# Kernel tuning notes

Hardware: AMD Instinct MI355X
Metric: run time of the kernel (lower is better)

Reference implementation:

```python
import jax, jax.numpy as jnp
import numpy as np

N = 55296      # nodes (C96 cubed-sphere)
B = 4          # batch
F = 64         # in_feats == out_feats
H = 256        # n_hidden
DEG = 4        # neighbors per node
E = N * DEG    # edges
NUM_STEP = 2


def setup_inputs() -> dict:
    key = jax.random.key(0)
    ks = jax.random.split(key, 24)
    inputs = jax.random.normal(ks[0], (B, N, F), jnp.float32)
    src = jax.random.randint(ks[1], (E,), 0, N, dtype=jnp.int32)
    dst = jnp.repeat(jnp.arange(N, dtype=jnp.int32), DEG)  # fixed in-degree 4
    d = {"inputs": inputs, "src": src, "dst": dst}
    # SAGEConv params: fc_self, fc_neigh, bias per layer
    dims = [(F, H), (H, H // 2), (H // 2, H // 4), (H // 4, H // 4), (H // 2, H // 2), (H, F)]
    for i, (di, do) in enumerate(dims, start=1):
        s = 1.0 / np.sqrt(di)
        d[f"ws{i}"] = jax.random.uniform(ks[3 * i], (di, do), jnp.float32, -s, s)
        d[f"wn{i}"] = jax.random.uniform(ks[3 * i + 1], (di, do), jnp.float32, -s, s)
        d[f"b{i}"] = jnp.zeros((do,), jnp.float32)
    return d


def _sage(x, src, dst, inv_deg, ws, wn, b):
    # x: [N, B, Fin] -> gather src endpoints, mean-aggregate onto dst nodes
    agg = jax.ops.segment_sum(x[src], dst, num_segments=N) * inv_deg  # [N, B, Fin]
    return jnp.einsum('nbf,fo->nbo', x, ws) + jnp.einsum('nbf,fo->nbo', agg, wn) + b


def reference(inputs, src, dst, ws1, wn1, b1, ws2, wn2, b2, ws3, wn3, b3,
              ws4, wn4, b4, ws5, wn5, b5, ws6, wn6, b6):
    deg = jax.ops.segment_sum(jnp.ones((E,), jnp.float32), dst, num_segments=N)
    inv_deg = (1.0 / jnp.maximum(deg, 1.0))[:, None, None]
    act = jax.nn.relu
    x = jnp.transpose(inputs, (1, 0, 2))  # [N, B, F]
    for _ in range(NUM_STEP):
        h1 = act(_sage(x, src, dst, inv_deg, ws1, wn1, b1))
        h2 = act(_sage(h1, src, dst, inv_deg, ws2, wn2, b2))
        h3 = act(_sage(h2, src, dst, inv_deg, ws3, wn3, b3))
        h4 = act(_sage(h3, src, dst, inv_deg, ws4, wn4, b4))
        h5 = jnp.concatenate([act(_sage(h4, src, dst, inv_deg, ws4, wn4, b4)), h3], axis=2)
        h6 = jnp.concatenate([act(_sage(h5, src, dst, inv_deg, ws5, wn5, b5)), h2], axis=2)
        x = _sage(h6, src, dst, inv_deg, ws6, wn6, b6)
    return jnp.transpose(x, (1, 0, 2))  # [B, N, F]
```

## Files before the change

kernel.cpp:

```cpp
#include <hip/hip_runtime.h>


#define NN 55296
#define MM (NN * 4)

typedef unsigned short u16;
typedef _Float16 f16;
typedef f16 f16x8 __attribute__((ext_vector_type(8)));
typedef float f32x4 __attribute__((ext_vector_type(4)));
typedef u16 u16x8 __attribute__((ext_vector_type(8)));

__device__ inline u16 f2h(float f) { return __builtin_bit_cast(u16, (f16)f); }
__device__ inline float h2f(u16 u) { return (float)__builtin_bit_cast(f16, u); }

__global__ __launch_bounds__(256) void k_fill(float* __restrict__ p, float v, int total) {
  int i = blockIdx.x * 256 + threadIdx.x;
  if (i < total) p[i] = v;
}

__global__ __launch_bounds__(256) void k_prep_x(const float* __restrict__ in,
                                                u16* __restrict__ out) {
  int idx = blockIdx.x * 256 + threadIdx.x;
  int n = idx >> 5, b = (idx >> 3) & 3, f0 = (idx & 7) * 8;
  const float* p = in + ((long)b * NN + n) * 64 + f0;
  float4 v0 = *(const float4*)p, v1 = *(const float4*)(p + 4);
  u16x8 r;
  r[0] = f2h(v0.x); r[1] = f2h(v0.y); r[2] = f2h(v0.z); r[3] = f2h(v0.w);
  r[4] = f2h(v1.x); r[5] = f2h(v1.y); r[6] = f2h(v1.z); r[7] = f2h(v1.w);
  *(u16x8*)(out + (((long)n * 4 + b) * 64 + f0)) = r;
}

__global__ __launch_bounds__(256) void k_prep_w(const float* __restrict__ wsrc,
                                                const float* __restrict__ wnsrc,
                                                int K, int N, u16* __restrict__ dst) {
  int idx = blockIdx.x * 256 + threadIdx.x;
  int K2 = 2 * K;
  if (idx >= N * K2) return;
  int n = idx / K2, k = idx - n * K2;
  float v = (k < K) ? wsrc[(long)k * N + n] : wnsrc[(long)(k - K) * N + n];
  dst[(long)n * K2 + k] = f2h(v);
}

__global__ __launch_bounds__(256) void k_prep_w2(const float* __restrict__ wsrc,
                                                 const float* __restrict__ wnsrc,
                                                 int K, int N, u16* __restrict__ dst) {
  int idx = blockIdx.x * 256 + threadIdx.x;
  int total = 2 * N * K;
  if (idx >= total) return;
  int r = idx / K, k = idx - r * K;
  float v = (r < N) ? wsrc[(long)k * N + r] : wnsrc[(long)k * N + (r - N)];
  dst[idx] = f2h(v);
}

template <int BM, int BN, int WM, int WN, typename TOUT, bool REMAP, bool GATHER>
__global__ __launch_bounds__(512, 4) void k_sage(
    const u16* __restrict__ X0, const u16* __restrict__ X1, int lda, int K0, int Ksum,
    const int4* __restrict__ src4, const u16* __restrict__ Wt,
    const float* __restrict__ bias, TOUT* __restrict__ OUT, long ldo,
    TOUT* __restrict__ OUT2, long ldo2, int Nsplit, int relu) {
  constexpr int GA = BM / 64;
  constexpr int GB = BN / 64;
  constexpr int NWM = BM / WM, NWN = BN / WN;
  static_assert(NWM * NWN == 8, "8 waves");
  constexpr int MF = WM / 16, NF = WN / 16;

  __shared__ __align__(16) u16 As[BM][64];
  __shared__ __align__(16) u16 Bs[BN][64];

  const int tid = threadIdx.x;
  const long m0 = (long)blockIdx.x * BM;
  const int n0 = blockIdx.y * BN;
  const int K2 = GATHER ? 2 * Ksum : Ksum;

  const int srow = tid >> 3;
  const int scg = tid & 7;

  int o_self[GA], o_g[GA][4];
#pragma unroll
  for (int i = 0; i < GA; ++i) {
    long m = m0 + srow + 64 * i;
    o_self[i] = (int)(m * lda);
    if constexpr (GATHER) {
      int b = (int)(m & 3);
      int4 s = src4[(int)(m >> 2)];
      o_g[i][0] = (s.x * 4 + b) * lda;
      o_g[i][1] = (s.y * 4 + b) * lda;
      o_g[i][2] = (s.z * 4 + b) * lda;
      o_g[i][3] = (s.w * 4 + b) * lda;
    }
  }
  long o_b[GB];
#pragma unroll
  for (int j = 0; j < GB; ++j) o_b[j] = (long)(n0 + srow + 64 * j) * K2 + scg * 8;

  u16x8 ra[GA][4];
  u16x8 rb[GB];

  const int w = tid >> 6, lane = tid & 63;
  const int wm = w % NWM, wn = w / NWM;
  const int mo = wm * WM, no = wn * WN;
  const int lr = lane & 15, lg = lane >> 4;

  f32x4 acc[MF][NF];
#pragma unroll
  for (int i = 0; i < MF; ++i)
#pragma unroll
    for (int j = 0; j < NF; ++j) {
      f32x4 z = {0.f, 0.f, 0.f, 0.f};
      acc[i][j] = z;
    }

  auto issue = [&](int kt) {
    const bool agg = GATHER && (kt >= Ksum);
    int cs = agg ? kt - Ksum : kt;
    const u16* Xp = X0;
    if (cs >= K0) { Xp = X1; cs -= K0; }
    const int cb = cs + scg * 8;
#pragma unroll
    for (int i = 0; i < GA; ++i) {
      if (agg) {
#pragma unroll
        for (int k = 0; k < 4; ++k)
          ra[i][k] = *(const u16x8*)(Xp + (long)o_g[i][k] + cb);
      } else {
        ra[i][0] = *(const u16x8*)(Xp + (long)o_self[i] + cb);
      }
    }
#pragma unroll
    for (int j = 0; j < GB; ++j)
      rb[j] = *(const u16x8*)(Wt + o_b[j] + kt);
  };
  auto commit = [&](bool agg) {
#pragma unroll
    for (int i = 0; i < GA; ++i) {
      const int row = srow + 64 * i;
      u16x8 v = ra[i][0];
      if (agg) {
        f16x8 s01 = __builtin_bit_cast(f16x8, ra[i][0]) + __builtin_bit_cast(f16x8, ra[i][1]);
        f16x8 s23 = __builtin_bit_cast(f16x8, ra[i][2]) + __builtin_bit_cast(f16x8, ra[i][3]);
        v = __builtin_bit_cast(u16x8, (s01 + s23) * (f16)0.25f);
      }
      *(u16x8*)&As[row][(scg ^ (row & 7)) * 8] = v;
    }
#pragma unroll
    for (int j = 0; j < GB; ++j) {
      const int row = srow + 64 * j;
      *(u16x8*)&Bs[row][(scg ^ (row & 7)) * 8] = rb[j];
    }
  };

  issue(0);
  for (int kt = 0; kt < K2; kt += 64) {
    commit(GATHER && kt >= Ksum);
    __syncthreads();
    const int nx = kt + 64;
    if (nx < K2) issue(nx);
#pragma unroll
    for (int ks = 0; ks < 2; ++ks) {
      f16x8 af[MF], bfr[NF];
#pragma unroll
      for (int i = 0; i < MF; ++i) {
        const int row = mo + i * 16 + lr;
        af[i] = __builtin_bit_cast(f16x8,
                  *(const u16x8*)&As[row][((ks * 4 + lg) ^ (row & 7)) * 8]);
      }
#pragma unroll
      for (int j = 0; j < NF; ++j) {
        const int row = no + j * 16 + lr;
        bfr[j] = __builtin_bit_cast(f16x8,
                   *(const u16x8*)&Bs[row][((ks * 4 + lg) ^ (row & 7)) * 8]);
      }
#pragma unroll
      for (int i = 0; i < MF; ++i)
#pragma unroll
        for (int j = 0; j < NF; ++j)
          acc[i][j] = __builtin_amdgcn_mfma_f32_16x16x32_f16(af[i], bfr[j], acc[i][j], 0, 0, 0);
    }
    __syncthreads();
  }

#pragma unroll
  for (int i = 0; i < MF; ++i)
#pragma unroll
    for (int j = 0; j < NF; ++j) {
      const int col = n0 + no + j * 16 + lr;
      const float bv = bias ? bias[col] : 0.f;
      TOUT* Op; long ld; int c;
      if (col < Nsplit) { Op = OUT; ld = ldo; c = col; }
      else              { Op = OUT2; ld = ldo2; c = col - Nsplit; }
#pragma unroll
      for (int r = 0; r < 4; ++r) {
        float v = acc[i][j][r] + bv;
        if (relu) v = fmaxf(v, 0.f);
        const long m = m0 + mo + i * 16 + lg * 4 + r;
        const long orow = REMAP ? ((m & 3) * (long)NN + (m >> 2)) : m;
        if constexpr (sizeof(TOUT) == 2) Op[orow * ld + c] = (TOUT)f2h(v);
        else                             Op[orow * ld + c] = v;
      }
    }
}

template <int N1, int KS1, int K2B, int N2, int NSPLIT>
__global__ __launch_bounds__(512, 4) void k_fuse2(
    const u16* __restrict__ X0, const u16* __restrict__ X1, int lda, int K0,
    const int4* __restrict__ src4,
    const u16* __restrict__ W1t, const float* __restrict__ bias1,
    const u16* __restrict__ G2, int ldg2,
    const u16* __restrict__ W2t,
    u16* __restrict__ OUT, long ldo, u16* __restrict__ OUT2, long ldo2) {
  constexpr int K21 = 2 * KS1;
  constexpr int K22 = N1 + K2B;
  constexpr int GB1 = N1 / 64, GB2 = N2 / 64;
  constexpr int BSROWS = (N1 > N2 ? N1 : N2);
  __shared__ __align__(16) u16 T[64][N1];
  __shared__ __align__(16) u16 As[64][64];
  __shared__ __align__(16) u16 Bs[BSROWS][64];

  const int tid = threadIdx.x;
  const long m0 = (long)blockIdx.x * 64;
  const int srow = tid >> 3, scg = tid & 7;
  const long mrow = m0 + srow;

  const int o_self = (int)(mrow * lda);
  const int bb = (int)(mrow & 3);
  const int4 s = src4[(int)(mrow >> 2)];
  const int og0 = (s.x * 4 + bb) * lda, og1 = (s.y * 4 + bb) * lda;
  const int og2 = (s.z * 4 + bb) * lda, og3 = (s.w * 4 + bb) * lda;

  const int w = tid >> 6, lane = tid & 63;
  const int lr = lane & 15, lg = lane >> 4;

  constexpr int NWN1 = N1 / 32, NWM1 = 8 / NWN1, WM1 = 64 / NWM1, MF1 = WM1 / 16;
  const int mo1 = (w % NWM1) * WM1, no1 = (w / NWM1) * 32;

  int ob1[GB1];
#pragma unroll
  for (int j = 0; j < GB1; ++j) ob1[j] = (srow + 64 * j) * K21 + scg * 8;

  u16x8 ra0, ra1, ra2, ra3, rb[GB1];

  auto issue1 = [&](int kt) {
    const bool agg = kt >= KS1;
    int cs = agg ? kt - KS1 : kt;
    const u16* Xp = X0;
    if (cs >= K0) { Xp = X1; cs -= K0; }
    const int cb = cs + scg * 8;
    if (agg) {
      ra0 = *(const u16x8*)(Xp + og0 + cb);
      ra1 = *(const u16x8*)(Xp + og1 + cb);
      ra2 = *(const u16x8*)(Xp + og2 + cb);
      ra3 = *(const u16x8*)(Xp + og3 + cb);
    } else {
      ra0 = *(const u16x8*)(Xp + o_self + cb);
    }
#pragma unroll
    for (int j = 0; j < GB1; ++j)
      rb[j] = *(const u16x8*)(W1t + ob1[j] + kt);
  };
  auto commit1 = [&](bool agg) {
    u16x8 v = ra0;
    if (agg) {
      f16x8 s01 = __builtin_bit_cast(f16x8, ra0) + __builtin_bit_cast(f16x8, ra1);
      f16x8 s23 = __builtin_bit_cast(f16x8, ra2) + __builtin_bit_cast(f16x8, ra3);
      v = __builtin_bit_cast(u16x8, (s01 + s23) * (f16)0.25f);
    }
    *(u16x8*)&As[srow][(scg ^ (srow & 7)) * 8] = v;
#pragma unroll
    for (int j = 0; j < GB1; ++j) {
      const int row = srow + 64 * j;
      *(u16x8*)&Bs[row][(scg ^ (row & 7)) * 8] = rb[j];
    }
  };

  f32x4 acc1[MF1][2];
#pragma unroll
  for (int i = 0; i < MF1; ++i) {
    f32x4 z = {0.f, 0.f, 0.f, 0.f};
    acc1[i][0] = z; acc1[i][1] = z;
  }

  issue1(0);
  for (int kt = 0; kt < K21; kt += 64) {
    commit1(kt >= KS1);
    __syncthreads();
    if (kt + 64 < K21) issue1(kt + 64);
#pragma unroll
    for (int ks = 0; ks < 2; ++ks) {
      f16x8 af[MF1], bf0, bf1;
#pragma unroll
      for (int i = 0; i < MF1; ++i) {
        const int row = mo1 + i * 16 + lr;
        af[i] = __builtin_bit_cast(f16x8,
                  *(const u16x8*)&As[row][((ks * 4 + lg) ^ (row & 7)) * 8]);
      }
      {
        const int row = no1 + lr;
        bf0 = __builtin_bit_cast(f16x8,
                *(const u16x8*)&Bs[row][((ks * 4 + lg) ^ (row & 7)) * 8]);
      }
      {
        const int row = no1 + 16 + lr;
        bf1 = __builtin_bit_cast(f16x8,
                *(const u16x8*)&Bs[row][((ks * 4 + lg) ^ (row & 7)) * 8]);
      }
#pragma unroll
      for (int i = 0; i < MF1; ++i) {
        acc1[i][0] = __builtin_amdgcn_mfma_f32_16x16x32_f16(af[i], bf0, acc1[i][0], 0, 0, 0);
        acc1[i][1] = __builtin_amdgcn_mfma_f32_16x16x32_f16(af[i], bf1, acc1[i][1], 0, 0, 0);
      }
    }
    __syncthreads();
  }

#pragma unroll
  for (int i = 0; i < MF1; ++i)
#pragma unroll
    for (int j = 0; j < 2; ++j) {
      const int col = no1 + j * 16 + lr;
      const float bv = bias1[col];
#pragma unroll
      for (int r = 0; r < 4; ++r) {
        float v = fmaxf(acc1[i][j][r] + bv, 0.f);
        const int row = mo1 + i * 16 + lg * 4 + r;
        T[row][(((col >> 3) ^ (row & 7)) << 3) | (col & 7)] = f2h(v);
      }
    }

  constexpr int NWN2 = N2 / 32, NWM2 = 8 / NWN2, WM2 = 64 / NWM2, MF2 = WM2 / 16;
  const int mo2 = (w % NWM2) * WM2, no2 = (w / NWM2) * 32;

  int ob2[GB2];
#pragma unroll
  for (int j = 0; j < GB2; ++j) ob2[j] = (srow + 64 * j) * K22 + scg * 8;
  const long oG = (K2B > 0) ? (mrow * (long)ldg2 + scg * 8) : 0;

  u16x8 rb2[GB2], rg;

  auto issue2 = [&](int kt) {
#pragma unroll
    for (int j = 0; j < GB2; ++j)
      rb2[j] = *(const u16x8*)(W2t + ob2[j] + kt);
    if constexpr (K2B > 0) {
      if (kt >= N1) rg = *(const u16x8*)(G2 + oG + (kt - N1));
    }
  };
  auto commit2 = [&](int kt) {
#pragma unroll
    for (int j = 0; j < GB2; ++j) {
      const int row = srow + 64 * j;
      *(u16x8*)&Bs[row][(scg ^ (row & 7)) * 8] = rb2[j];
    }
    if constexpr (K2B > 0) {
      if (kt >= N1) *(u16x8*)&As[srow][(scg ^ (srow & 7)) * 8] = rg;
    }
  };

  f32x4 acc2[MF2][2];
#pragma unroll
  for (int i = 0; i < MF2; ++i) {
    f32x4 z = {0.f, 0.f, 0.f, 0.f};
    acc2[i][0] = z; acc2[i][1] = z;
  }

  issue2(0);
  for (int kt = 0; kt < K22; kt += 64) {
    commit2(kt);
    __syncthreads();
    if (kt + 64 < K22) issue2(kt + 64);
    const bool fromT = kt < N1;
#pragma unroll
    for (int ks = 0; ks < 2; ++ks) {
      f16x8 af[MF2], bf0, bf1;
#pragma unroll
      for (int i = 0; i < MF2; ++i) {
        const int row = mo2 + i * 16 + lr;
        if (fromT) {
          const int g = (kt >> 3) + ks * 4 + lg;
          af[i] = __builtin_bit_cast(f16x8,
                    *(const u16x8*)&T[row][(g ^ (row & 7)) * 8]);
        } else {
          af[i] = __builtin_bit_cast(f16x8,
                    *(const u16x8*)&As[row][((ks * 4 + lg) ^ (row & 7)) * 8]);
        }
      }
      {
        const int row = no2 + lr;
        bf0 = __builtin_bit_cast(f16x8,
                *(const u16x8*)&Bs[row][((ks * 4 + lg) ^ (row & 7)) * 8]);
      }
      {
        const int row = no2 + 16 + lr;
        bf1 = __builtin_bit_cast(f16x8,
                *(const u16x8*)&Bs[row][((ks * 4 + lg) ^ (row & 7)) * 8]);
      }
#pragma unroll
      for (int i = 0; i < MF2; ++i) {
        acc2[i][0] = __builtin_amdgcn_mfma_f32_16x16x32_f16(af[i], bf0, acc2[i][0], 0, 0, 0);
        acc2[i][1] = __builtin_amdgcn_mfma_f32_16x16x32_f16(af[i], bf1, acc2[i][1], 0, 0, 0);
      }
    }
    __syncthreads();
  }

#pragma unroll
  for (int i = 0; i < MF2; ++i)
#pragma unroll
    for (int j = 0; j < 2; ++j) {
      const int col = no2 + j * 16 + lr;
      u16* Op; long ld; int c;
      if (col < NSPLIT) { Op = OUT; ld = ldo; c = col; }
      else              { Op = OUT2; ld = ldo2; c = col - NSPLIT; }
#pragma unroll
      for (int r = 0; r < 4; ++r) {
        const long m = m0 + mo2 + i * 16 + lg * 4 + r;
        Op[m * ld + c] = f2h(acc2[i][j][r]);
      }
    }
}

template <typename TOUT, bool REMAP, bool RELU, int GSH>
__global__ __launch_bounds__(256) void k_gadd(
    const u16* __restrict__ Y, long ldy, const u16* __restrict__ Z, long ldz,
    const int4* __restrict__ src4, const float* __restrict__ bias,
    TOUT* __restrict__ OUT, long ldo) {
  const int idx = blockIdx.x * 256 + threadIdx.x;
  const int g = idx & ((1 << GSH) - 1);
  const long m = idx >> GSH;
  const int b = (int)(m & 3), n = (int)(m >> 2);
  const int4 s = src4[n];
  u16x8 ys = *(const u16x8*)(Y + m * ldy + g * 8);
  u16x8 z0 = *(const u16x8*)(Z + (long)(s.x * 4 + b) * ldz + g * 8);
  u16x8 z1 = *(const u16x8*)(Z + (long)(s.y * 4 + b) * ldz + g * 8);
  u16x8 z2 = *(const u16x8*)(Z + (long)(s.z * 4 + b) * ldz + g * 8);
  u16x8 z3 = *(const u16x8*)(Z + (long)(s.w * 4 + b) * ldz + g * 8);
  float4 bv0 = *(const float4*)(bias + g * 8);
  float4 bv1 = *(const float4*)(bias + g * 8 + 4);
  float o[8];
#pragma unroll
  for (int j = 0; j < 8; ++j) {
    float bj = (j < 4) ? (&bv0.x)[j] : (&bv1.x)[j - 4];
    float v = h2f(ys[j]) + 0.25f * (h2f(z0[j]) + h2f(z1[j]) + h2f(z2[j]) + h2f(z3[j])) + bj;
    o[j] = RELU ? fmaxf(v, 0.f) : v;
  }
  const long orow = REMAP ? ((long)b * NN + n) : m;
  if constexpr (sizeof(TOUT) == 2) {
    u16x8 r;
#pragma unroll
    for (int j = 0; j < 8; ++j) r[j] = f2h(o[j]);
    *(u16x8*)(OUT + orow * ldo + g * 8) = r;
  } else {
#pragma unroll
    for (int j = 0; j < 8; ++j) OUT[orow * ldo + g * 8 + j] = o[j];
  }
}

extern "C" void kernel_launch(void* const* d_in, const int* in_sizes, int n_in,
                              void* d_out, int out_size, void* d_ws, size_t ws_size,
                              hipStream_t stream) {
  const float* inputs = (const float*)d_in[0];
  const int*   src    = (const int*)d_in[1];
  const float* W[6][3];
  for (int i = 0; i < 6; ++i) {
    W[i][0] = (const float*)d_in[3 + 3 * i];
    W[i][1] = (const float*)d_in[4 + 3 * i];
    W[i][2] = (const float*)d_in[5 + 3 * i];
  }

  const long M = (long)MM;
  const int dims[6][2] = {{64,256},{256,128},{128,64},{64,64},{128,128},{256,64}};
  long wo[6]; long wtot = 0;
  for (int i = 0; i < 6; ++i) { wo[i] = wtot; wtot += (long)dims[i][1] * 2 * dims[i][0]; }

  const size_t needed = ((size_t)384 * M + wtot) * sizeof(u16);
  if (ws_size < needed) {
    float mb = (float)(ws_size >> 20);
    k_fill<<<(out_size + 255) / 256, 256, 0, stream>>>((float*)d_out, mb, out_size);
    return;
  }

  u16* act = (u16*)d_ws;
  u16* Y1  = act + 0 * M;
  u16* H2  = act + 0 * M;
  u16* Z1  = act + 128 * M;
  u16* YZ2 = act + 128 * M;
  u16* H5a = act + 128 * M;
  u16* Y6  = act + 192 * M;
  u16* H3  = act + 256 * M;
  u16* Xb  = act + 320 * M;
  u16* H4  = act + 320 * M;
  u16* Z6  = act + 320 * M;
  u16* WT  = act + 384 * M;
  u16* Xp  = (u16*)d_out;
  const int4* src4 = (const int4*)src;

  k_prep_x<<<NN * 32 / 256, 256, 0, stream>>>(inputs, Xb);
  for (int i : {0, 3, 4}) {
    int total = dims[i][1] * 2 * dims[i][0];
    k_prep_w<<<(total + 255) / 256, 256, 0, stream>>>(W[i][0], W[i][1], dims[i][0],
                                                      dims[i][1], WT + wo[i]);
  }
  for (int i : {1, 2, 5}) {
    int total = 2 * dims[i][1] * dims[i][0];
    k_prep_w2<<<(total + 255) / 256, 256, 0, stream>>>(W[i][0], W[i][1], dims[i][0],
                                                       dims[i][1], WT + wo[i]);
  }

  const int BIG = 1 << 30;
  const dim3 g1(MM / 128, 1);
  for (int step = 0; step < 2; ++step) {
    const u16* x0 = step ? Xp : Xb;
    k_fuse2<256, 64, 0, 256, 128><<<MM / 64, 512, 0, stream>>>(
        x0, x0, 64, 64, src4, WT + wo[0], W[0][2],
        nullptr, 0, WT + wo[1], Y1, 128, Z1, 128);
    k_gadd<u16, false, true, 4><<<MM * 16 / 256, 256, 0, stream>>>(
        Y1, 128, Z1, 128, src4, W[1][2], H2, 128);
    k_sage<128, 128, 64, 32, u16, false, false><<<g1, 512, 0, stream>>>(
        H2, H2, 128, 128, 128, src4, WT + wo[2], nullptr, YZ2, 128,
        (u16*)nullptr, 0, BIG, 0);
    k_gadd<u16, false, true, 3><<<MM * 8 / 256, 256, 0, stream>>>(
        YZ2, 128, YZ2 + 64, 128, src4, W[2][2], H3, 64);
    k_sage<128, 64, 32, 32, u16, false, true><<<g1, 512, 0, stream>>>(
        H3, H3, 64, 64, 64, src4, WT + wo[3], W[3][2], H4, 64,
        (u16*)nullptr, 0, BIG, 1);
    k_sage<128, 64, 32, 32, u16, false, true><<<g1, 512, 0, stream>>>(
        H4, H4, 64, 64, 64, src4, WT + wo[3], W[3][2], H5a, 64,
        (u16*)nullptr, 0, BIG, 1);
    k_fuse2<128, 128, 128, 128, 64><<<MM / 64, 512, 0, stream>>>(
        H5a, H3, 64, 64, src4, WT + wo[4], W[4][2],
        H2, 128, WT + wo[5], Y6, 64, Z6, 64);
    if (step == 0)
      k_gadd<u16, false, false, 3><<<MM * 8 / 256, 256, 0, stream>>>(
          Y6, 64, Z6, 64, src4, W[5][2], Xp, 64);
    else
      k_gadd<float, true, false, 3><<<MM * 8 / 256, 256, 0, stream>>>(
          Y6, 64, Z6, 64, src4, W[5][2], (float*)d_out, 64);
  }
}
```

Measured before the change: 655.0 us.

## Load second-GEMM weight fragments directly into registers, merging shared buffers

In the fused two-GEMM kernel, the second GEMM now reads its weight B-fragments straight from global memory into registers with double buffering, instead of staging them through shared memory. This removes most of the per-k-step barriers, since only the G2 tiles still pass through the As buffer. The separate T and Bs shared arrays are merged into one BT buffer, which lowers LDS use and may raise occupancy. In exchange, every wave reloads the weights from global/L2 without reuse across waves, and the extra registers held for the fragments and rg tiles can add register pressure.

```diff
diff --git a/kernel.cpp b/kernel.cpp
--- a/kernel.cpp
+++ b/kernel.cpp
@@ -210,11 +210,10 @@
     u16* __restrict__ OUT, long ldo, u16* __restrict__ OUT2, long ldo2) {
   constexpr int K21 = 2 * KS1;
   constexpr int K22 = N1 + K2B;
-  constexpr int GB1 = N1 / 64, GB2 = N2 / 64;
-  constexpr int BSROWS = (N1 > N2 ? N1 : N2);
-  __shared__ __align__(16) u16 T[64][N1];
+  constexpr int GB1 = N1 / 64;
+  constexpr int NG2 = (K2B > 0) ? K2B / 64 : 1;
+  __shared__ __align__(16) u16 BT[64 * N1];
   __shared__ __align__(16) u16 As[64][64];
-  __shared__ __align__(16) u16 Bs[BSROWS][64];
 
   const int tid = threadIdx.x;
   const long m0 = (long)blockIdx.x * 64;
@@ -268,7 +267,7 @@
 #pragma unroll
     for (int j = 0; j < GB1; ++j) {
       const int row = srow + 64 * j;
-      *(u16x8*)&Bs[row][(scg ^ (row & 7)) * 8] = rb[j];
+      *(u16x8*)&BT[row * 64 + (scg ^ (row & 7)) * 8] = rb[j];
     }
   };
 
@@ -296,12 +295,12 @@
       {
         const int row = no1 + lr;
         bf0 = __builtin_bit_cast(f16x8,
-                *(const u16x8*)&Bs[row][((ks * 4 + lg) ^ (row & 7)) * 8]);
+                *(const u16x8*)&BT[row * 64 + ((ks * 4 + lg) ^ (row & 7)) * 8]);
       }
       {
         const int row = no1 + 16 + lr;
         bf1 = __builtin_bit_cast(f16x8,
-                *(const u16x8*)&Bs[row][((ks * 4 + lg) ^ (row & 7)) * 8]);
+                *(const u16x8*)&BT[row * 64 + ((ks * 4 + lg) ^ (row & 7)) * 8]);
       }
 #pragma unroll
       for (int i = 0; i < MF1; ++i) {
@@ -322,38 +321,21 @@
       for (int r = 0; r < 4; ++r) {
         float v = fmaxf(acc1[i][j][r] + bv, 0.f);
         const int row = mo1 + i * 16 + lg * 4 + r;
-        T[row][(((col >> 3) ^ (row & 7)) << 3) | (col & 7)] = f2h(v);
-      }
-    }
+        BT[row * N1 + ((((col >> 3) ^ (row & 7)) << 3) | (col & 7))] = f2h(v);
+      }
+    }
+
+  u16x8 rg[NG2];
+  if constexpr (K2B > 0) {
+    const long oG = mrow * (long)ldg2 + scg * 8;
+#pragma unroll
+    for (int t = 0; t < NG2; ++t)
+      rg[t] = *(const u16x8*)(G2 + oG + t * 64);
+  }
+  __syncthreads();
 
   constexpr int NWN2 = N2 / 32, NWM2 = 8 / NWN2, WM2 = 64 / NWM2, MF2 = WM2 / 16;
   const int mo2 = (w % NWM2) * WM2, no2 = (w / NWM2) * 32;
-
-  int ob2[GB2];
-#pragma unroll
-  for (int j = 0; j < GB2; ++j) ob2[j] = (srow + 64 * j) * K22 + scg * 8;
-  const long oG = (K2B > 0) ? (mrow * (long)ldg2 + scg * 8) : 0;
-
-  u16x8 rb2[GB2], rg;
-
-  auto issue2 = [&](int kt) {
-#pragma unroll
-    for (int j = 0; j < GB2; ++j)
-      rb2[j] = *(const u16x8*)(W2t + ob2[j] + kt);
-    if constexpr (K2B > 0) {
-      if (kt >= N1) rg = *(const u16x8*)(G2 + oG + (kt - N1));
-    }
-  };
-  auto commit2 = [&](int kt) {
-#pragma unroll
-    for (int j = 0; j < GB2; ++j) {
-      const int row = srow + 64 * j;
-      *(u16x8*)&Bs[row][(scg ^ (row & 7)) * 8] = rb2[j];
-    }
-    if constexpr (K2B > 0) {
-      if (kt >= N1) *(u16x8*)&As[srow][(scg ^ (srow & 7)) * 8] = rg;
-    }
-  };
 
   f32x4 acc2[MF2][2];
 #pragma unroll
@@ -362,44 +344,50 @@
     acc2[i][0] = z; acc2[i][1] = z;
   }
 
-  issue2(0);
+  u16x8 wf[2][2][2];
+  auto loadW = [&](int kt, int buf) {
+#pragma unroll
+    for (int j = 0; j < 2; ++j)
+#pragma unroll
+      for (int ks = 0; ks < 2; ++ks)
+        wf[buf][j][ks] = *(const u16x8*)(
+            W2t + (long)(no2 + j * 16 + lr) * K22 + kt + ks * 32 + lg * 8);
+  };
+
+  loadW(0, 0);
+#pragma unroll
   for (int kt = 0; kt < K22; kt += 64) {
-    commit2(kt);
-    __syncthreads();
-    if (kt + 64 < K22) issue2(kt + 64);
+    const int buf = (kt >> 6) & 1;
     const bool fromT = kt < N1;
+    if (!fromT) {
+      *(u16x8*)&As[srow][(scg ^ (srow & 7)) * 8] = rg[(kt - N1) >> 6];
+      __syncthreads();
+    }
+    if (kt + 64 < K22) loadW(kt + 64, buf ^ 1);
 #pragma unroll
     for (int ks = 0; ks < 2; ++ks) {
-      f16x8 af[MF2], bf0, bf1;
+      f16x8 af[MF2];
 #pragma unroll
       for (int i = 0; i < MF2; ++i) {
         const int row = mo2 + i * 16 + lr;
         if (fromT) {
           const int g = (kt >> 3) + ks * 4 + lg;
           af[i] = __builtin_bit_cast(f16x8,
-                    *(const u16x8*)&T[row][(g ^ (row & 7)) * 8]);
+                    *(const u16x8*)&BT[row * N1 + (g ^ (row & 7)) * 8]);
         } else {
           af[i] = __builtin_bit_cast(f16x8,
                     *(const u16x8*)&As[row][((ks * 4 + lg) ^ (row & 7)) * 8]);
         }
       }
-      {
-        const int row = no2 + lr;
-        bf0 = __builtin_bit_cast(f16x8,
-                *(const u16x8*)&Bs[row][((ks * 4 + lg) ^ (row & 7)) * 8]);
-      }
-      {
-        const int row = no2 + 16 + lr;
-        bf1 = __builtin_bit_cast(f16x8,
-                *(const u16x8*)&Bs[row][((ks * 4 + lg) ^ (row & 7)) * 8]);
-      }
 #pragma unroll
       for (int i = 0; i < MF2; ++i) {
-        acc2[i][0] = __builtin_amdgcn_mfma_f32_16x16x32_f16(af[i], bf0, acc2[i][0], 0, 0, 0);
-        acc2[i][1] = __builtin_amdgcn_mfma_f32_16x16x32_f16(af[i], bf1, acc2[i][1], 0, 0, 0);
-      }
-    }
-    __syncthreads();
+        acc2[i][0] = __builtin_amdgcn_mfma_f32_16x16x32_f16(
+            af[i], __builtin_bit_cast(f16x8, wf[buf][0][ks]), acc2[i][0], 0, 0, 0);
+        acc2[i][1] = __builtin_amdgcn_mfma_f32_16x16x32_f16(
+            af[i], __builtin_bit_cast(f16x8, wf[buf][1][ks]), acc2[i][1], 0, 0, 0);
+      }
+    }
+    if (!fromT) __syncthreads();
   }
 
 #pragma unroll
```

New measurement: 768.4 us. +17.3%, slower.

## Fuse layer-2 gather-add epilogue into layer-3 GEMM A-tile load

Applied to the files above, without the earlier changes.

Removes the separate k_gadd launch that built H2 from Y1 and gathered Z1. The layer-3 k_sage kernel (new GMODE==2) now loads Y1 rows plus four gathered Z1 neighbor rows, applies the mean, bias and ReLU in fp32, and writes the A tile to shared memory. It also stores H2 to global memory, since the skip connection later needs it. The workspace layout is reshuffled so that YZ2 lives in the output buffer, which avoids overlapping live buffers. This saves one full read/write pass of H2, at the cost of more scattered gather loads inside the GEMM and extra register pressure.

```diff
diff --git a/kernel.cpp b/kernel.cpp
--- a/kernel.cpp
+++ b/kernel.cpp
@@ -52,12 +52,14 @@
   dst[idx] = f2h(v);
 }
 
-template <int BM, int BN, int WM, int WN, typename TOUT, bool REMAP, bool GATHER>
+template <int BM, int BN, int WM, int WN, typename TOUT, bool REMAP, int GMODE>
 __global__ __launch_bounds__(512, 4) void k_sage(
     const u16* __restrict__ X0, const u16* __restrict__ X1, int lda, int K0, int Ksum,
     const int4* __restrict__ src4, const u16* __restrict__ Wt,
     const float* __restrict__ bias, TOUT* __restrict__ OUT, long ldo,
-    TOUT* __restrict__ OUT2, long ldo2, int Nsplit, int relu) {
+    TOUT* __restrict__ OUT2, long ldo2, int Nsplit, int relu,
+    const u16* __restrict__ Yg, const u16* __restrict__ Zg,
+    const float* __restrict__ biasg, u16* __restrict__ Hout) {
   constexpr int GA = BM / 64;
   constexpr int GB = BN / 64;
   constexpr int NWM = BM / WM, NWN = BN / WN;
@@ -70,31 +72,33 @@
   const int tid = threadIdx.x;
   const long m0 = (long)blockIdx.x * BM;
   const int n0 = blockIdx.y * BN;
-  const int K2 = GATHER ? 2 * Ksum : Ksum;
+  const int K2 = (GMODE == 1) ? 2 * Ksum : Ksum;
 
   const int srow = tid >> 3;
   const int scg = tid & 7;
 
-  int o_self[GA], o_g[GA][4];
+  long o_self[GA]; int o_g[GA][4];
 #pragma unroll
   for (int i = 0; i < GA; ++i) {
     long m = m0 + srow + 64 * i;
-    o_self[i] = (int)(m * lda);
-    if constexpr (GATHER) {
+    o_self[i] = m * ((GMODE == 2) ? 128 : lda);
+    if constexpr (GMODE != 0) {
       int b = (int)(m & 3);
       int4 s = src4[(int)(m >> 2)];
-      o_g[i][0] = (s.x * 4 + b) * lda;
-      o_g[i][1] = (s.y * 4 + b) * lda;
-      o_g[i][2] = (s.z * 4 + b) * lda;
-      o_g[i][3] = (s.w * 4 + b) * lda;
+      int ldg = (GMODE == 2) ? 128 : lda;
+      o_g[i][0] = (s.x * 4 + b) * ldg;
+      o_g[i][1] = (s.y * 4 + b) * ldg;
+      o_g[i][2] = (s.z * 4 + b) * ldg;
+      o_g[i][3] = (s.w * 4 + b) * ldg;
     }
   }
   long o_b[GB];
 #pragma unroll
   for (int j = 0; j < GB; ++j) o_b[j] = (long)(n0 + srow + 64 * j) * K2 + scg * 8;
 
-  u16x8 ra[GA][4];
+  u16x8 ra[GA][4], ry[GA < 1 ? 1 : GA];
   u16x8 rb[GB];
+  float4 rbv0, rbv1;
 
   const int w = tid >> 6, lane = tid & 63;
   const int wm = w % NWM, wn = w / NWM;
@@ -111,31 +115,55 @@
     }
 
   auto issue = [&](int kt) {
-    const bool agg = GATHER && (kt >= Ksum);
-    int cs = agg ? kt - Ksum : kt;
-    const u16* Xp = X0;
-    if (cs >= K0) { Xp = X1; cs -= K0; }
-    const int cb = cs + scg * 8;
-#pragma unroll
-    for (int i = 0; i < GA; ++i) {
-      if (agg) {
-#pragma unroll
-        for (int k = 0; k < 4; ++k)
-          ra[i][k] = *(const u16x8*)(Xp + (long)o_g[i][k] + cb);
-      } else {
-        ra[i][0] = *(const u16x8*)(Xp + (long)o_self[i] + cb);
+    if constexpr (GMODE == 2) {
+      const int cb = kt + scg * 8;
+#pragma unroll
+      for (int i = 0; i < GA; ++i) {
+        ry[i]    = *(const u16x8*)(Yg + o_self[i] + cb);
+        ra[i][0] = *(const u16x8*)(Zg + o_g[i][0] + cb);
+        ra[i][1] = *(const u16x8*)(Zg + o_g[i][1] + cb);
+        ra[i][2] = *(const u16x8*)(Zg + o_g[i][2] + cb);
+        ra[i][3] = *(const u16x8*)(Zg + o_g[i][3] + cb);
+      }
+      rbv0 = *(const float4*)(biasg + cb);
+      rbv1 = *(const float4*)(biasg + cb + 4);
+    } else {
+      const bool agg = (GMODE == 1) && (kt >= Ksum);
+      int cs = agg ? kt - Ksum : kt;
+      const u16* Xp = X0;
+      if (cs >= K0) { Xp = X1; cs -= K0; }
+      const int cb = cs + scg * 8;
+#pragma unroll
+      for (int i = 0; i < GA; ++i) {
+        if (agg) {
+#pragma unroll
+          for (int k = 0; k < 4; ++k)
+            ra[i][k] = *(const u16x8*)(Xp + o_g[i][k] + cb);
+        } else {
+          ra[i][0] = *(const u16x8*)(Xp + o_self[i] + cb);
+        }
       }
     }
 #pragma unroll
     for (int j = 0; j < GB; ++j)
       rb[j] = *(const u16x8*)(Wt + o_b[j] + kt);
   };
-  auto commit = [&](bool agg) {
+  auto commit = [&](int kt) {
 #pragma unroll
     for (int i = 0; i < GA; ++i) {
       const int row = srow + 64 * i;
       u16x8 v = ra[i][0];
-      if (agg) {
+      if constexpr (GMODE == 2) {
+#pragma unroll
+        for (int j = 0; j < 8; ++j) {
+          float bj = (j < 4) ? (&rbv0.x)[j] : (&rbv1.x)[j - 4];
+          float t = h2f(ry[i][j]) +
+                    0.25f * (h2f(ra[i][0][j]) + h2f(ra[i][1][j]) +
+                             h2f(ra[i][2][j]) + h2f(ra[i][3][j])) + bj;
+          v[j] = f2h(fmaxf(t, 0.f));
+        }
+        *(u16x8*)(Hout + (m0 + row) * 128 + kt + scg * 8) = v;
+      } else if (GMODE == 1 && kt >= Ksum) {
         f16x8 s01 = __builtin_bit_cast(f16x8, ra[i][0]) + __builtin_bit_cast(f16x8, ra[i][1]);
         f16x8 s23 = __builtin_bit_cast(f16x8, ra[i][2]) + __builtin_bit_cast(f16x8, ra[i][3]);
         v = __builtin_bit_cast(u16x8, (s01 + s23) * (f16)0.25f);
@@ -151,7 +179,7 @@
 
   issue(0);
   for (int kt = 0; kt < K2; kt += 64) {
-    commit(GATHER && kt >= Ksum);
+    commit(kt);
     __syncthreads();
     const int nx = kt + 64;
     if (nx < K2) issue(nx);
@@ -395,8 +423,10 @@
       }
 #pragma unroll
       for (int i = 0; i < MF2; ++i) {
-        acc2[i][0] = __builtin_amdgcn_mfma_f32_16x16x32_f16(af[i], bf0, acc2[i][0], 0, 0, 0);
-        acc2[i][1] = __builtin_amdgcn_mfma_f32_16x16x32_f16(af[i], bf1, acc2[i][1], 0, 0, 0);
+        acc2[i][0] = __builtin_amdgcn_mfma_f32_16x16x32_f16(
+            af[i], __builtin_bit_cast(f16x8, bf0), acc2[i][0], 0, 0, 0);
+        acc2[i][1] = __builtin_amdgcn_mfma_f32_16x16x32_f16(
+            af[i], __builtin_bit_cast(f16x8, bf1), acc2[i][1], 0, 0, 0);
       }
     }
     __syncthreads();
@@ -480,16 +510,16 @@
 
   u16* act = (u16*)d_ws;
   u16* Y1  = act + 0 * M;
-  u16* H2  = act + 0 * M;
+  u16* H3  = act + 0 * M;
+  u16* H4  = act + 64 * M;
+  u16* Z6  = act + 64 * M;
   u16* Z1  = act + 128 * M;
-  u16* YZ2 = act + 128 * M;
   u16* H5a = act + 128 * M;
   u16* Y6  = act + 192 * M;
-  u16* H3  = act + 256 * M;
-  u16* Xb  = act + 320 * M;
-  u16* H4  = act + 320 * M;
-  u16* Z6  = act + 320 * M;
+  u16* Xb  = act + 256 * M;
+  u16* H2  = act + 256 * M;
   u16* WT  = act + 384 * M;
+  u16* YZ2 = (u16*)d_out;
   u16* Xp  = (u16*)d_out;
   const int4* src4 = (const int4*)src;
 
@@ -512,19 +542,17 @@
     k_fuse2<256, 64, 0, 256, 128><<<MM / 64, 512, 0, stream>>>(
         x0, x0, 64, 64, src4, WT + wo[0], W[0][2],
         nullptr, 0, WT + wo[1], Y1, 128, Z1, 128);
-    k_gadd<u16, false, true, 4><<<MM * 16 / 256, 256, 0, stream>>>(
-        Y1, 128, Z1, 128, src4, W[1][2], H2, 128);
-    k_sage<128, 128, 64, 32, u16, false, false><<<g1, 512, 0, stream>>>(
-        H2, H2, 128, 128, 128, src4, WT + wo[2], nullptr, YZ2, 128,
-        (u16*)nullptr, 0, BIG, 0);
+    k_sage<128, 128, 64, 32, u16, false, 2><<<g1, 512, 0, stream>>>(
+        Y1, Y1, 128, 128, 128, src4, WT + wo[2], nullptr, YZ2, 128,
+        (u16*)nullptr, 0, BIG, 0, Y1, Z1, W[1][2], H2);
     k_gadd<u16, false, true, 3><<<MM * 8 / 256, 256, 0, stream>>>(
         YZ2, 128, YZ2 + 64, 128, src4, W[2][2], H3, 64);
-    k_sage<128, 64, 32, 32, u16, false, true><<<g1, 512, 0, stream>>>(
+    k_sage<128, 64, 32, 32, u16, false, 1><<<g1, 512, 0, stream>>>(
         H3, H3, 64, 64, 64, src4, WT + wo[3], W[3][2], H4, 64,
-        (u16*)nullptr, 0, BIG, 1);
-    k_sage<128, 64, 32, 32, u16, false, true><<<g1, 512, 0, stream>>>(
+        (u16*)nullptr, 0, BIG, 1, nullptr, nullptr, nullptr, nullptr);
+    k_sage<128, 64, 32, 32, u16, false, 1><<<g1, 512, 0, stream>>>(
         H4, H4, 64, 64, 64, src4, WT + wo[3], W[3][2], H5a, 64,
-        (u16*)nullptr, 0, BIG, 1);
+        (u16*)nullptr, 0, BIG, 1, nullptr, nullptr, nullptr, nullptr);
     k_fuse2<128, 128, 128, 128, 64><<<MM / 64, 512, 0, stream>>>(
         H5a, H3, 64, 64, src4, WT + wo[4], W[4][2],
         H2, 128, WT + wo[5], Y6, 64, Z6, 64);
```

After: 734.3 us. +12.1%, slower.
